# Performance work log

Hardware: AMD Instinct MI355X
Metric: run time of the kernel (lower is better)

## Reference

```python
import jax, jax.numpy as jnp
import numpy as np

H, W = 160, 160
FS = 7
SPAN = FS // 2
NUM_CLASSES = 19
NUM_ITERS = 5
THETA_ALPHA = 160.0  # scales rgb in bilateral features
THETA_BETA = 3.0     # scales position in bilateral features
THETA_GAMMA = 3.0    # scales position in spatial features
EPS = 1e-20

# offsets ordered (dx outer, dy inner) to match TF filter-tap index (dx+span)*FS + (dy+span)
OFFSETS = [(dx, dy) for dx in range(-SPAN, SPAN + 1) for dy in range(-SPAN, SPAN + 1)]


def _make_filter(features):
    # features: (bs, cf, H, W) -> gaussian affinity filter (bs, FS*FS, H, W)
    # filter[b, k, i, j] = exp(-0.5 * ||f[b,:,i+dx,j+dy] - f[b,:,i,j]||^2), 0 if out of bounds
    fp = jnp.pad(features, ((0, 0), (0, 0), (SPAN, SPAN), (SPAN, SPAN)))
    rows = jnp.arange(H)
    cols = jnp.arange(W)
    taps = []
    for dx, dy in OFFSETS:
        shifted = fp[:, :, SPAN + dx:SPAN + dx + H, SPAN + dy:SPAN + dy + W]
        aff = jnp.exp(-0.5 * jnp.sum((features - shifted) ** 2, axis=1))  # (bs, H, W)
        mask = (((rows + dx >= 0) & (rows + dx < H))[:, None]
                & ((cols + dy >= 0) & (cols + dy < W))[None, :])
        taps.append(aff * mask)
    return jnp.stack(taps, axis=1)  # (bs, FS*FS, H, W)


def _patches(x):
    # x: (bs, C, H, W) -> (bs, C, FS*FS, H, W), zero-padded shifts (matches extract_patches SAME)
    xp = jnp.pad(x, ((0, 0), (0, 0), (SPAN, SPAN), (SPAN, SPAN)))
    return jnp.stack(
        [xp[:, :, SPAN + dx:SPAN + dx + H, SPAN + dy:SPAN + dy + W] for dx, dy in OFFSETS],
        axis=2)


def _compute_gaussian(x, filt):
    # x: (bs, C, H, W), filt: (bs, FS*FS, H, W) -> (bs, C, H, W)
    return jnp.sum(_patches(x) * filt[:, None], axis=2)


def _forward(unaries, rgb, spatial_ker_weights, bilateral_ker_weights, compatibility_matrix):
    u = jnp.transpose(unaries, (0, 3, 1, 2))     # (bs, C, H, W)
    rgb_nchw = jnp.transpose(rgb, (0, 3, 1, 2))  # (bs, 3, H, W)
    bs = u.shape[0]
    mesh = jnp.stack(
        jnp.meshgrid(jnp.arange(H, dtype=jnp.float32), jnp.arange(W, dtype=jnp.float32),
                     indexing='ij'), 0)          # (2, H, W)
    spatial_feat = jnp.broadcast_to((mesh / THETA_GAMMA)[None], (bs, 2, H, W))
    bilateral_feat = jnp.concatenate(
        [rgb_nchw / THETA_ALPHA,
         jnp.broadcast_to((mesh / THETA_BETA)[None], (bs, 2, H, W))], axis=1)  # (bs, 5, H, W)

    spatial_filter = _make_filter(spatial_feat)
    bilateral_filter = _make_filter(bilateral_feat)

    ones = jnp.ones_like(u)
    spatial_norm = _compute_gaussian(ones, spatial_filter)
    bilateral_norm = _compute_gaussian(ones, bilateral_filter)

    q = u
    for _ in range(NUM_ITERS):
        # NOTE: original code does tf.nn.softmax(q_values, 0) -> softmax over the BATCH axis.
        sm = jax.nn.softmax(q, axis=0)
        s_out = _compute_gaussian(sm, spatial_filter) / (spatial_norm + EPS)
        b_out = _compute_gaussian(sm, bilateral_filter) / (bilateral_norm + EPS)
        msg = (jnp.einsum('kc,bchw->bkhw', spatial_ker_weights, s_out)
               + jnp.einsum('kc,bchw->bkhw', bilateral_ker_weights, b_out))
        pairwise = jnp.einsum('kc,bchw->bkhw', compatibility_matrix, msg)
        q = u - pairwise
    return jnp.transpose(q, (0, 2, 3, 1))  # (bs, H, W, C)


def setup_inputs() -> dict:
    key = jax.random.key(0)
    k1, k2 = jax.random.split(key)
    unaries = jax.random.normal(k1, (2, H, W, NUM_CLASSES), dtype=jnp.float32)
    rgb = jax.random.uniform(k2, (2, H, W, 3), dtype=jnp.float32) * 255.0
    eye = jnp.eye(NUM_CLASSES, dtype=jnp.float32)
    return {
        'unaries': unaries,
        'rgb': rgb,
        'spatial_ker_weights': eye,            # _diagonal_initializer
        'bilateral_ker_weights': eye,          # _diagonal_initializer
        'compatibility_matrix': -eye,          # _potts_model_initializer
    }


def reference(unaries, rgb, spatial_ker_weights, bilateral_ker_weights, compatibility_matrix):
    return _forward(unaries, rgb, spatial_ker_weights, bilateral_ker_weights,
                    compatibility_matrix)
```

## Files before the change

### kernel.cpp

```cpp
#include <hip/hip_runtime.h>


typedef __attribute__((ext_vector_type(4))) _Float16 half4;
typedef __attribute__((ext_vector_type(2))) _Float16 half2f;
typedef __attribute__((ext_vector_type(4))) float float4v;

#define HH 160
#define WW 160
#define NPIX (HH*WW)
#define NC 19
#define NG 5
#define SPAN 3
#define TR 8
#define TC 16
#define NPXT 128
#define LR 14
#define LC 22
#define LCP 24
#define HSTRIDE (LR*LCP)
#define LCP_F 25
#define HS_F (LR*LCP_F)
#define NHALO (LR*LC)
#define NRING 180
#define NBLK 200
#define NTHR 640
#define EPSF 1e-20f

#define EPTAG   0x5EED0000u
#define EPMASK  0xFFFF0000u

#define EPW(b) (32 + (b)*32)

#define SZ_A    30720
#define OFF_WB  SZ_A
#define PN_OFF  20480
#define SHM_SZ  (SZ_A + 25*128*8)

__device__ __forceinline__ float fast_rcp(float x) { return __builtin_amdgcn_rcpf(x); }

__device__ __forceinline__ float smx0(float q0, float q1) {
    const float m  = fmaxf(q0, q1);
    const float e0 = __expf(q0 - m);
    const float e1 = __expf(q1 - m);
    return e0 * fast_rcp(e0 + e1);
}

__device__ __forceinline__ unsigned ep_decode(unsigned w) {
    return ((w & EPMASK) == EPTAG) ? (w & 0xFFFFu) : 0u;
}

__global__ void __launch_bounds__(NTHR) crf_kernel(
        const float* __restrict__ u,
        const float* __restrict__ rgb,
        const float* __restrict__ sw,
        const float* __restrict__ bw,
        const float* __restrict__ compat,
        unsigned long long* __restrict__ gsmA,
        unsigned long long* __restrict__ gsmB,
        unsigned* __restrict__ bar,
        float* __restrict__ out) {
    __shared__ __align__(16) char shm[SHM_SZ];
    __shared__ float Msh[960];
    __shared__ float rowsum[NC];
    __shared__ int   diagflag;
    float4*   rgbL = (float4*)shm;
    float4v*  smF  = (float4v*)shm;
    float*    accF = (float*)shm;
    unsigned* wbW  = (unsigned*)(shm + OFF_WB);
    const uint2* wbP = (const uint2*)(shm + OFF_WB);

    constexpr float WSPC[49] = {
        0.36787944f,0.48567179f,0.57375342f,0.60653066f,0.57375342f,0.48567179f,0.36787944f,
        0.48567179f,0.64118039f,0.75746513f,0.80073740f,0.75746513f,0.64118039f,0.48567179f,
        0.57375342f,0.75746513f,0.89483932f,0.94595947f,0.89483932f,0.75746513f,0.57375342f,
        0.60653066f,0.80073740f,0.94595947f,1.00000000f,0.94595947f,0.80073740f,0.60653066f,
        0.57375342f,0.75746513f,0.89483932f,0.94595947f,0.89483932f,0.75746513f,0.57375342f,
        0.48567179f,0.64118039f,0.75746513f,0.80073740f,0.75746513f,0.64118039f,0.48567179f,
        0.36787944f,0.48567179f,0.57375342f,0.60653066f,0.57375342f,0.48567179f,0.36787944f };

    const int tid = threadIdx.x;
    const int px  = tid & 127;
    const int g   = tid >> 7;
    const int r   = px >> 4, c = px & 15;
    const int ti0 = blockIdx.y * TR, tj0 = blockIdx.x * TC;
    const int gp  = (ti0 + r) * WW + (tj0 + c);
    const int ctr  = (r + SPAN) * LCP   + (c + SPAN);
    const int ctrF = (r + SPAN) * LCP_F + (c + SPAN);
    const int ku  = 4 * g;
    const int bid = blockIdx.y * 10 + blockIdx.x;

    int nb[8];
    {
        const int bx = blockIdx.x, by = blockIdx.y;
        int k = 0;
        #pragma unroll
        for (int dy2 = -1; dy2 <= 1; ++dy2)
            #pragma unroll
            for (int dx2 = -1; dx2 <= 1; ++dx2) {
                if (dx2 == 0 && dy2 == 0) continue;
                const int nx = bx + dx2, ny = by + dy2;
                nb[k++] = ((unsigned)nx < 10u && (unsigned)ny < 20u) ? (ny*10 + nx) : bid;
            }
    }

    if (tid == 0) diagflag = 1;

    float uv0[4], uv1[4];
    #pragma unroll
    for (int i = 0; i < 4; ++i) {
        const int ch = 4*g + i;
        uv0[i] = (ch < NC) ? u[(size_t)gp * NC + ch] : 0.0f;
        uv1[i] = (ch < NC) ? u[((size_t)NPIX + gp) * NC + ch] : 0.0f;
    }
    half4 sh;
    float smv[4];
    #pragma unroll
    for (int i = 0; i < 4; ++i) {
        smv[i] = smx0(uv0[i], uv1[i]);
        sh[i]  = (_Float16)smv[i];
    }
    {
        unsigned long long u64; __builtin_memcpy(&u64, &sh, 8);
        __hip_atomic_store(&gsmA[g * NPIX + gp], u64,
                           __ATOMIC_RELAXED, __HIP_MEMORY_SCOPE_AGENT);
    }

    if (tid < NC) {
        float rs = 0.0f;
        for (int cb = 0; cb < NC; ++cb) rs += sw[tid*NC + cb] + bw[tid*NC + cb];
        rowsum[tid] = rs;
    }
    __syncthreads();
    if (tid == 0)
        __hip_atomic_store(&bar[EPW(bid)], EPTAG | 1u,
                           __ATOMIC_RELAXED, __HIP_MEMORY_SCOPE_AGENT);

    float4 rv;
    int rgb_idx = -1;
    if (tid < 2 * NHALO) {
        const int bb = tid / NHALO, pos = tid % NHALO;
        const int hr = pos / LC, hc = pos % LC;
        const int yi = ti0 - SPAN + hr, xj = tj0 - SPAN + hc;
        rv = make_float4(0.f, 0.f, 0.f, 0.f);
        if ((unsigned)yi < HH && (unsigned)xj < WW) {
            const float* p = rgb + ((size_t)(bb * NPIX) + yi * WW + xj) * 3;
            rv = make_float4(p[0]*(1.f/160.f), p[1]*(1.f/160.f), p[2]*(1.f/160.f), 1.f);
        }
        rgb_idx = (bb ? HSTRIDE : 0) + hr * LCP + hc;
    }

    for (int e = tid; e < 960; e += NTHR) {
        const int k = e / 48, cc2 = e % 48;
        float acc = 0.0f;
        if (k < NC) {
            if (cc2 < NC) {
                for (int j = 0; j < NC; ++j) acc += compat[k*NC + j] * sw[j*NC + cc2];
            } else if (cc2 >= 20 && cc2 < 20 + NC) {
                const int cb = cc2 - 20;
                for (int j = 0; j < NC; ++j) acc += compat[k*NC + j] * bw[j*NC + cb];
            } else if (cc2 == 40) {
                for (int j = 0; j < NC; ++j) acc += compat[k*NC + j] * rowsum[j];
            }
        }
        Msh[e] = acc;
        bool off = false;
        if (k < NC) {
            if (cc2 < NC && cc2 != k && acc != 0.0f) off = true;
            if (cc2 >= 20 && cc2 < 20 + NC && (cc2 - 20) != k && acc != 0.0f) off = true;
        }
        if (off) atomicAnd(&diagflag, 0);
    }

    if (rgb_idx >= 0) rgbL[rgb_idx] = rv;
    __syncthreads();

    float dsv[4], dbv[4];
    #pragma unroll
    for (int i = 0; i < 4; ++i) {
        dsv[i] = Msh[(ku + i) * 48 + (ku + i)];
        dbv[i] = Msh[(ku + i) * 48 + 20 + (ku + i)];
    }
    const bool isdiag = (diagflag != 0);

    {
        const float4 cv0 = rgbL[ctr];
        const float4 cv1 = rgbL[HSTRIDE + ctr];
        const int tapb = g * 10;
        const int ntap = (g == 4) ? 9 : 10;
        float pn0 = 0.f, pn1 = 0.f;
        for (int i = 0; i < ntap; ++i) {
            const int t = tapb + i;
            const int dx = t / 7 - SPAN, dy = t % 7 - SPAN;
            const int n = ctr + dx * LCP + dy;
            const float4 nv0 = rgbL[n];
            const float4 nv1 = rgbL[HSTRIDE + n];
            const float spc = (float)(dx*dx + dy*dy) * (-1.f/18.f);
            const float dr0 = cv0.x-nv0.x, dg0 = cv0.y-nv0.y, db0 = cv0.z-nv0.z;
            const float dr1 = cv1.x-nv1.x, dg1 = cv1.y-nv1.y, db1 = cv1.z-nv1.z;
            const float d0 = dr0*dr0 + dg0*dg0 + db0*db0;
            const float d1 = dr1*dr1 + dg1*dg1 + db1*db1;
            const float wb0 = nv0.w * __expf(fmaf(d0, -0.5f, spc));
            const float wb1 = nv0.w * __expf(fmaf(d1, -0.5f, spc));
            half2f hw = {(_Float16)wb0, (_Float16)wb1};
            unsigned uw; __builtin_memcpy(&uw, &hw, 4);
            wbW[(t >> 1) * 256 + px * 2 + (t & 1)] = uw;
            pn0 += (float)hw.x; pn1 += (float)hw.y;
        }
        if (g == 4) wbW[24 * 256 + px * 2 + 1] = 0u;
        *(float2*)(shm + PN_OFF + (g * 128 + px) * 8) = make_float2(pn0, pn1);
    }
    __syncthreads();

    float snI, bnI0, bnI1;
    {
        float bn0 = 0.f, bn1 = 0.f;
        #pragma unroll
        for (int g2 = 0; g2 < 5; ++g2) {
            const float2 p = *(const float2*)(shm + PN_OFF + (g2 * 128 + px) * 8);
            bn0 += p.x; bn1 += p.y;
        }
        const int rg = ti0 + r, cg = tj0 + c;
        float Rr = 5.70645506f, Cc = 5.70645506f;
        Rr -= (rg < 3   ? 0.60653066f : 0.f) + (rg < 2   ? 0.80073740f : 0.f)
            + (rg < 1   ? 0.94595947f : 0.f) + (rg > 156 ? 0.60653066f : 0.f)
            + (rg > 157 ? 0.80073740f : 0.f) + (rg > 158 ? 0.94595947f : 0.f);
        Cc -= (cg < 3   ? 0.60653066f : 0.f) + (cg < 2   ? 0.80073740f : 0.f)
            + (cg < 1   ? 0.94595947f : 0.f) + (cg > 156 ? 0.60653066f : 0.f)
            + (cg > 157 ? 0.80073740f : 0.f) + (cg > 158 ? 0.94595947f : 0.f);
        snI  = fast_rcp(Rr * Cc + EPSF);
        bnI0 = fast_rcp(bn0 + EPSF);
        bnI1 = fast_rcp(bn1 + EPSF);
    }

    for (int it = 0; it < 5; ++it) {
        __syncthreads();

        {
            const float4v sv = {smv[0], smv[1], smv[2], smv[3]};
            smF[g * HS_F + ctrF] = sv;
        }

        if (tid == 0) {
            const unsigned seq = (unsigned)(it + 1);
            if (it > 0)
                __hip_atomic_store(&bar[EPW(bid)], EPTAG | seq,
                                   __ATOMIC_RELAXED, __HIP_MEMORY_SCOPE_AGENT);
            unsigned mn;
            do {
                mn = 0xFFFFu;
                #pragma unroll
                for (int k = 0; k < 8; ++k) {
                    const unsigned w = __hip_atomic_load(&bar[EPW(nb[k])],
                                                         __ATOMIC_RELAXED, __HIP_MEMORY_SCOPE_AGENT);
                    const unsigned e = ep_decode(w);
                    mn = (e < mn) ? e : mn;
                }
                if (mn < seq) __builtin_amdgcn_s_sleep(1);
            } while (mn < seq);
        }
        __syncthreads();

        const unsigned long long* gsrc = ((it & 1) ? gsmB : gsmA);
        #pragma unroll
        for (int k2 = 0; k2 < 2; ++k2) {
            const int e = tid + NTHR * k2;
            if (e < NG * NRING) {
                const int sg = e / NRING, re = e - sg * NRING;
                int hr, hc;
                if (re < 66)        { hr = re / 22;          hc = re % 22; }
                else if (re < 132)  { const int t2 = re - 66;  hr = 11 + t2 / 22; hc = t2 % 22; }
                else                { const int t2 = re - 132; hr = 3 + t2 / 6;
                                      const int s = t2 % 6;    hc = (s < 3) ? s : s + 16; }
                const int yi = ti0 - SPAN + hr, xj = tj0 - SPAN + hc;
                float4v fv = (float4v)0.0f;
                if ((unsigned)yi < HH && (unsigned)xj < WW) {
                    const unsigned long long raw =
                        __hip_atomic_load(&gsrc[sg * NPIX + yi * WW + xj],
                                          __ATOMIC_RELAXED, __HIP_MEMORY_SCOPE_AGENT);
                    half4 hv; __builtin_memcpy(&hv, &raw, 8);
                    fv = (float4v){(float)hv[0], (float)hv[1], (float)hv[2], (float)hv[3]};
                }
                smF[sg * HS_F + hr * LCP_F + hc] = fv;
            }
        }
        __syncthreads();

        float4v sAv = (float4v)0.0f, b0a = (float4v)0.0f, b1a = (float4v)0.0f;
        const float4v* pl = smF + g * HS_F;
        #pragma unroll
        for (int i = 0; i < 24; ++i) {
            const uint2 wp = wbP[i * 128 + px];
            #pragma unroll
            for (int s = 0; s < 2; ++s) {
                const int t = 2*i + s;
                const int dx = t / 7 - SPAN, dy = t % 7 - SPAN;
                half2f hw; __builtin_memcpy(&hw, s ? &wp.y : &wp.x, 4);
                const float w0 = (float)hw.x, w1 = (float)hw.y;
                const float4v f = pl[ctrF + dx*LCP_F + dy];
                sAv += WSPC[t] * f;
                b0a += w0 * f;
                b1a += w1 * f;
            }
        }
        {
            const uint2 wp = wbP[24 * 128 + px];
            half2f hw; __builtin_memcpy(&hw, &wp.x, 4);
            const float w0 = (float)hw.x, w1 = (float)hw.y;
            const float4v f = pl[ctrF + SPAN*LCP_F + SPAN];
            sAv += WSPC[48] * f;
            b0a += w0 * f;
            b1a += w1 * f;
        }

        float q0v[4], q1v[4];
        if (isdiag) {
            #pragma unroll
            for (int i = 0; i < 4; ++i) {
                const float sAn = sAv[i] * snI;
                const float b0n = b0a[i] * bnI0;
                const float b1x = b1a[i] * bnI1;
                q0v[i] = uv0[i] - dsv[i]*sAn - dbv[i]*b0n;
                q1v[i] = uv1[i] - (dsv[i] + dbv[i]) + dsv[i]*sAn + dbv[i]*b1x;
            }
        } else {
            __syncthreads();
            #pragma unroll
            for (int i = 0; i < 4; ++i) {
                accF[(4*g + i) * NPXT + px]      = sAv[i] * snI;
                accF[(20 + 4*g + i) * NPXT + px] = b0a[i] * bnI0;
                accF[(40 + 4*g + i) * NPXT + px] = b1a[i] * bnI1;
            }
            __syncthreads();
            float t1[4] = {0,0,0,0}, t2[4] = {0,0,0,0}, t3[4] = {0,0,0,0};
            #pragma unroll
            for (int cc = 0; cc < 20; ++cc) {
                const float sv  = accF[cc * NPXT + px];
                const float b0v = accF[(20 + cc) * NPXT + px];
                const float b1v = accF[(40 + cc) * NPXT + px];
                #pragma unroll
                for (int i = 0; i < 4; ++i) {
                    const float* mk = Msh + (ku + i) * 48;
                    t1[i] += mk[cc] * sv;
                    t2[i] += mk[20 + cc] * b0v;
                    t3[i] += mk[20 + cc] * b1v;
                }
            }
            #pragma unroll
            for (int i = 0; i < 4; ++i) {
                const float rs = Msh[(ku + i) * 48 + 40];
                q0v[i] = uv0[i] - t1[i] - t2[i];
                q1v[i] = uv1[i] - rs + t1[i] + t3[i];
            }
        }

        if (it == 4) {
            #pragma unroll
            for (int i = 0; i < 4; ++i) {
                const int ch = 4*g + i;
                if (ch < NC) {
                    out[(size_t)gp * NC + ch]          = q0v[i];
                    out[((size_t)NPIX + gp) * NC + ch] = q1v[i];
                }
            }
        } else {
            #pragma unroll
            for (int i = 0; i < 4; ++i) {
                smv[i] = smx0(q0v[i], q1v[i]);
                sh[i]  = (_Float16)smv[i];
            }
            unsigned long long u64; __builtin_memcpy(&u64, &sh, 8);
            unsigned long long* gdst = (((it + 1) & 1) ? gsmB : gsmA);
            __hip_atomic_store(&gdst[g * NPIX + gp], u64,
                               __ATOMIC_RELAXED, __HIP_MEMORY_SCOPE_AGENT);
        }
    }
}

extern "C" void kernel_launch(void* const* d_in, const int* in_sizes, int n_in,
                              void* d_out, int out_size, void* d_ws, size_t ws_size,
                              hipStream_t stream) {
    const float* u      = (const float*)d_in[0];
    const float* rgb    = (const float*)d_in[1];
    const float* sw     = (const float*)d_in[2];
    const float* bw     = (const float*)d_in[3];
    const float* compat = (const float*)d_in[4];
    float* out = (float*)d_out;

    unsigned long long* gsmA = (unsigned long long*)d_ws;
    unsigned long long* gsmB = (unsigned long long*)((char*)d_ws + 1024000);
    unsigned* bar = (unsigned*)((char*)d_ws + 2048000);

    crf_kernel<<<dim3(WW/TC, HH/TR, 1), dim3(NTHR), 0, stream>>>(
        u, rgb, sw, bw, compat, gsmA, gsmB, bar, out);
}
```

Measured before the change: 101.9 us.

## Retile to 10x10 pixel blocks over a 16x16 grid of 256 blocks

Changes the spatial tile from 8x16 to 10x10 pixels, giving 256 persistent blocks of 512 threads (500 active) instead of 200 blocks of 640. The halo, ring-exchange indexing, shared-memory strides and neighbour barrier are adjusted to match. The intent is to fill all 256 CUs of the MI355X so each neighbour-synchronized iteration finishes sooner. In exchange the halo-to-interior ratio rises, 12 threads per block sit idle, and the barrier spin now gives up after a bounded count, which could break the synchronization if a neighbour is very slow.

```diff
diff --git a/kernel.cpp b/kernel.cpp
--- a/kernel.cpp
+++ b/kernel.cpp
@@ -11,19 +11,18 @@
 #define NC 19
 #define NG 5
 #define SPAN 3
-#define TR 8
-#define TC 16
-#define NPXT 128
-#define LR 14
-#define LC 22
-#define LCP 24
+#define TR 10
+#define TC 10
+#define NPXT 100
+#define LR 16
+#define LC 16
+#define LCP 17
 #define HSTRIDE (LR*LCP)
-#define LCP_F 25
-#define HS_F (LR*LCP_F)
 #define NHALO (LR*LC)
-#define NRING 180
-#define NBLK 200
-#define NTHR 640
+#define NRING 156
+#define NBLK 256
+#define NTHR 512
+#define NACT 500
 #define EPSF 1e-20f
 
 #define EPTAG   0x5EED0000u
@@ -31,10 +30,10 @@
 
 #define EPW(b) (32 + (b)*32)
 
-#define SZ_A    30720
+#define SZ_A    24064
+#define PN_OFF  8704
 #define OFF_WB  SZ_A
-#define PN_OFF  20480
-#define SHM_SZ  (SZ_A + 25*128*8)
+#define SHM_SZ  (SZ_A + 20000)
 
 __device__ __forceinline__ float fast_rcp(float x) { return __builtin_amdgcn_rcpf(x); }
 
@@ -79,15 +78,15 @@
         0.36787944f,0.48567179f,0.57375342f,0.60653066f,0.57375342f,0.48567179f,0.36787944f };
 
     const int tid = threadIdx.x;
-    const int px  = tid & 127;
-    const int g   = tid >> 7;
-    const int r   = px >> 4, c = px & 15;
+    const bool act = (tid < NACT);
+    const int g   = tid / NPXT;
+    const int px  = tid - g * NPXT;
+    const int r   = px / TC, c = px - r * TC;
     const int ti0 = blockIdx.y * TR, tj0 = blockIdx.x * TC;
     const int gp  = (ti0 + r) * WW + (tj0 + c);
-    const int ctr  = (r + SPAN) * LCP   + (c + SPAN);
-    const int ctrF = (r + SPAN) * LCP_F + (c + SPAN);
+    const int ctr = (r + SPAN) * LCP + (c + SPAN);
     const int ku  = 4 * g;
-    const int bid = blockIdx.y * 10 + blockIdx.x;
+    const int bid = blockIdx.y * 16 + blockIdx.x;
 
     int nb[8];
     {
@@ -99,27 +98,27 @@
             for (int dx2 = -1; dx2 <= 1; ++dx2) {
                 if (dx2 == 0 && dy2 == 0) continue;
                 const int nx = bx + dx2, ny = by + dy2;
-                nb[k++] = ((unsigned)nx < 10u && (unsigned)ny < 20u) ? (ny*10 + nx) : bid;
+                nb[k++] = ((unsigned)nx < 16u && (unsigned)ny < 16u) ? (ny*16 + nx) : bid;
             }
     }
 
     if (tid == 0) diagflag = 1;
 
     float uv0[4], uv1[4];
-    #pragma unroll
-    for (int i = 0; i < 4; ++i) {
-        const int ch = 4*g + i;
-        uv0[i] = (ch < NC) ? u[(size_t)gp * NC + ch] : 0.0f;
-        uv1[i] = (ch < NC) ? u[((size_t)NPIX + gp) * NC + ch] : 0.0f;
-    }
     half4 sh;
     float smv[4];
-    #pragma unroll
-    for (int i = 0; i < 4; ++i) {
-        smv[i] = smx0(uv0[i], uv1[i]);
-        sh[i]  = (_Float16)smv[i];
-    }
-    {
+    if (act) {
+        #pragma unroll
+        for (int i = 0; i < 4; ++i) {
+            const int ch = 4*g + i;
+            uv0[i] = (ch < NC) ? u[(size_t)gp * NC + ch] : 0.0f;
+            uv1[i] = (ch < NC) ? u[((size_t)NPIX + gp) * NC + ch] : 0.0f;
+        }
+        #pragma unroll
+        for (int i = 0; i < 4; ++i) {
+            smv[i] = smx0(uv0[i], uv1[i]);
+            sh[i]  = (_Float16)smv[i];
+        }
         unsigned long long u64; __builtin_memcpy(&u64, &sh, 8);
         __hip_atomic_store(&gsmA[g * NPIX + gp], u64,
                            __ATOMIC_RELAXED, __HIP_MEMORY_SCOPE_AGENT);
@@ -136,17 +135,17 @@
                            __ATOMIC_RELAXED, __HIP_MEMORY_SCOPE_AGENT);
 
     float4 rv;
-    int rgb_idx = -1;
-    if (tid < 2 * NHALO) {
-        const int bb = tid / NHALO, pos = tid % NHALO;
-        const int hr = pos / LC, hc = pos % LC;
+    int rgb_idx;
+    {
+        const int bb = tid >> 8, pos = tid & 255;
+        const int hr = pos >> 4, hc = pos & 15;
         const int yi = ti0 - SPAN + hr, xj = tj0 - SPAN + hc;
         rv = make_float4(0.f, 0.f, 0.f, 0.f);
         if ((unsigned)yi < HH && (unsigned)xj < WW) {
             const float* p = rgb + ((size_t)(bb * NPIX) + yi * WW + xj) * 3;
             rv = make_float4(p[0]*(1.f/160.f), p[1]*(1.f/160.f), p[2]*(1.f/160.f), 1.f);
         }
-        rgb_idx = (bb ? HSTRIDE : 0) + hr * LCP + hc;
+        rgb_idx = bb * HSTRIDE + hr * LCP + hc;
     }
 
     for (int e = tid; e < 960; e += NTHR) {
@@ -171,7 +170,7 @@
         if (off) atomicAnd(&diagflag, 0);
     }
 
-    if (rgb_idx >= 0) rgbL[rgb_idx] = rv;
+    rgbL[rgb_idx] = rv;
     __syncthreads();
 
     float dsv[4], dbv[4];
@@ -182,7 +181,7 @@
     }
     const bool isdiag = (diagflag != 0);
 
-    {
+    if (act) {
         const float4 cv0 = rgbL[ctr];
         const float4 cv1 = rgbL[HSTRIDE + ctr];
         const int tapb = g * 10;
@@ -203,20 +202,20 @@
             const float wb1 = nv0.w * __expf(fmaf(d1, -0.5f, spc));
             half2f hw = {(_Float16)wb0, (_Float16)wb1};
             unsigned uw; __builtin_memcpy(&uw, &hw, 4);
-            wbW[(t >> 1) * 256 + px * 2 + (t & 1)] = uw;
+            wbW[(t >> 1) * 200 + px * 2 + (t & 1)] = uw;
             pn0 += (float)hw.x; pn1 += (float)hw.y;
         }
-        if (g == 4) wbW[24 * 256 + px * 2 + 1] = 0u;
-        *(float2*)(shm + PN_OFF + (g * 128 + px) * 8) = make_float2(pn0, pn1);
+        if (g == 4) wbW[24 * 200 + px * 2 + 1] = 0u;
+        *(float2*)(shm + PN_OFF + (g * NPXT + px) * 8) = make_float2(pn0, pn1);
     }
     __syncthreads();
 
     float snI, bnI0, bnI1;
-    {
+    if (act) {
         float bn0 = 0.f, bn1 = 0.f;
         #pragma unroll
         for (int g2 = 0; g2 < 5; ++g2) {
-            const float2 p = *(const float2*)(shm + PN_OFF + (g2 * 128 + px) * 8);
+            const float2 p = *(const float2*)(shm + PN_OFF + (g2 * NPXT + px) * 8);
             bn0 += p.x; bn1 += p.y;
         }
         const int rg = ti0 + r, cg = tj0 + c;
@@ -235,9 +234,9 @@
     for (int it = 0; it < 5; ++it) {
         __syncthreads();
 
-        {
+        if (act) {
             const float4v sv = {smv[0], smv[1], smv[2], smv[3]};
-            smF[g * HS_F + ctrF] = sv;
+            smF[g * HSTRIDE + ctr] = sv;
         }
 
         if (tid == 0) {
@@ -246,6 +245,7 @@
                 __hip_atomic_store(&bar[EPW(bid)], EPTAG | seq,
                                    __ATOMIC_RELAXED, __HIP_MEMORY_SCOPE_AGENT);
             unsigned mn;
+            unsigned spins = 0;
             do {
                 mn = 0xFFFFu;
                 #pragma unroll
@@ -255,7 +255,10 @@
                     const unsigned e = ep_decode(w);
                     mn = (e < mn) ? e : mn;
                 }
-                if (mn < seq) __builtin_amdgcn_s_sleep(1);
+                if (mn < seq) {
+                    __builtin_amdgcn_s_sleep(1);
+                    if (++spins > (1u << 22)) break;
+                }
             } while (mn < seq);
         }
         __syncthreads();
@@ -267,10 +270,10 @@
             if (e < NG * NRING) {
                 const int sg = e / NRING, re = e - sg * NRING;
                 int hr, hc;
-                if (re < 66)        { hr = re / 22;          hc = re % 22; }
-                else if (re < 132)  { const int t2 = re - 66;  hr = 11 + t2 / 22; hc = t2 % 22; }
-                else                { const int t2 = re - 132; hr = 3 + t2 / 6;
-                                      const int s = t2 % 6;    hc = (s < 3) ? s : s + 16; }
+                if (re < 48)        { hr = re >> 4;               hc = re & 15; }
+                else if (re < 96)   { hr = 13 + ((re - 48) >> 4); hc = (re - 48) & 15; }
+                else                { const int t2 = re - 96; hr = 3 + t2 / 6;
+                                      const int s = t2 % 6;   hc = (s < 3) ? s : s + 10; }
                 const int yi = ti0 - SPAN + hr, xj = tj0 - SPAN + hc;
                 float4v fv = (float4v)0.0f;
                 if ((unsigned)yi < HH && (unsigned)xj < WW) {
@@ -280,89 +283,99 @@
                     half4 hv; __builtin_memcpy(&hv, &raw, 8);
                     fv = (float4v){(float)hv[0], (float)hv[1], (float)hv[2], (float)hv[3]};
                 }
-                smF[sg * HS_F + hr * LCP_F + hc] = fv;
+                smF[sg * HSTRIDE + hr * LCP + hc] = fv;
             }
         }
         __syncthreads();
 
         float4v sAv = (float4v)0.0f, b0a = (float4v)0.0f, b1a = (float4v)0.0f;
-        const float4v* pl = smF + g * HS_F;
-        #pragma unroll
-        for (int i = 0; i < 24; ++i) {
-            const uint2 wp = wbP[i * 128 + px];
+        if (act) {
+            const float4v* pl = smF + g * HSTRIDE;
             #pragma unroll
-            for (int s = 0; s < 2; ++s) {
-                const int t = 2*i + s;
-                const int dx = t / 7 - SPAN, dy = t % 7 - SPAN;
-                half2f hw; __builtin_memcpy(&hw, s ? &wp.y : &wp.x, 4);
+            for (int i = 0; i < 24; ++i) {
+                const uint2 wp = wbP[i * 100 + px];
+                #pragma unroll
+                for (int s = 0; s < 2; ++s) {
+                    const int t = 2*i + s;
+                    const int dx = t / 7 - SPAN, dy = t % 7 - SPAN;
+                    half2f hw; __builtin_memcpy(&hw, s ? &wp.y : &wp.x, 4);
+                    const float w0 = (float)hw.x, w1 = (float)hw.y;
+                    const float4v f = pl[ctr + dx*LCP + dy];
+                    sAv += WSPC[t] * f;
+                    b0a += w0 * f;
+                    b1a += w1 * f;
+                }
+            }
+            {
+                const uint2 wp = wbP[24 * 100 + px];
+                half2f hw; __builtin_memcpy(&hw, &wp.x, 4);
                 const float w0 = (float)hw.x, w1 = (float)hw.y;
-                const float4v f = pl[ctrF + dx*LCP_F + dy];
-                sAv += WSPC[t] * f;
+                const float4v f = pl[ctr + SPAN*LCP + SPAN];
+                sAv += WSPC[48] * f;
                 b0a += w0 * f;
                 b1a += w1 * f;
             }
         }
-        {
-            const uint2 wp = wbP[24 * 128 + px];
-            half2f hw; __builtin_memcpy(&hw, &wp.x, 4);
-            const float w0 = (float)hw.x, w1 = (float)hw.y;
-            const float4v f = pl[ctrF + SPAN*LCP_F + SPAN];
-            sAv += WSPC[48] * f;
-            b0a += w0 * f;
-            b1a += w1 * f;
-        }
 
         float q0v[4], q1v[4];
         if (isdiag) {
-            #pragma unroll
-            for (int i = 0; i < 4; ++i) {
-                const float sAn = sAv[i] * snI;
-                const float b0n = b0a[i] * bnI0;
-                const float b1x = b1a[i] * bnI1;
-                q0v[i] = uv0[i] - dsv[i]*sAn - dbv[i]*b0n;
-                q1v[i] = uv1[i] - (dsv[i] + dbv[i]) + dsv[i]*sAn + dbv[i]*b1x;
+            if (act) {
+                #pragma unroll
+                for (int i = 0; i < 4; ++i) {
+                    const float sAn = sAv[i] * snI;
+                    const float b0n = b0a[i] * bnI0;
+                    const float b1x = b1a[i] * bnI1;
+                    q0v[i] = uv0[i] - dsv[i]*sAn - dbv[i]*b0n;
+                    q1v[i] = uv1[i] - (dsv[i] + dbv[i]) + dsv[i]*sAn + dbv[i]*b1x;
+                }
             }
         } else {
             __syncthreads();
-            #pragma unroll
-            for (int i = 0; i < 4; ++i) {
-                accF[(4*g + i) * NPXT + px]      = sAv[i] * snI;
-                accF[(20 + 4*g + i) * NPXT + px] = b0a[i] * bnI0;
-                accF[(40 + 4*g + i) * NPXT + px] = b1a[i] * bnI1;
+            if (act) {
+                #pragma unroll
+                for (int i = 0; i < 4; ++i) {
+                    accF[(4*g + i) * NPXT + px]      = sAv[i] * snI;
+                    accF[(20 + 4*g + i) * NPXT + px] = b0a[i] * bnI0;
+                    accF[(40 + 4*g + i) * NPXT + px] = b1a[i] * bnI1;
+                }
             }
             __syncthreads();
-            float t1[4] = {0,0,0,0}, t2[4] = {0,0,0,0}, t3[4] = {0,0,0,0};
-            #pragma unroll
-            for (int cc = 0; cc < 20; ++cc) {
-                const float sv  = accF[cc * NPXT + px];
-                const float b0v = accF[(20 + cc) * NPXT + px];
-                const float b1v = accF[(40 + cc) * NPXT + px];
+            if (act) {
+                float t1[4] = {0,0,0,0}, t2[4] = {0,0,0,0}, t3[4] = {0,0,0,0};
+                #pragma unroll
+                for (int cc = 0; cc < 20; ++cc) {
+                    const float sv  = accF[cc * NPXT + px];
+                    const float b0v = accF[(20 + cc) * NPXT + px];
+                    const float b1v = accF[(40 + cc) * NPXT + px];
+                    #pragma unroll
+                    for (int i = 0; i < 4; ++i) {
+                        const float* mk = Msh + (ku + i) * 48;
+                        t1[i] += mk[cc] * sv;
+                        t2[i] += mk[20 + cc] * b0v;
+                        t3[i] += mk[20 + cc] * b1v;
+                    }
+                }
                 #pragma unroll
                 for (int i = 0; i < 4; ++i) {
-                    const float* mk = Msh + (ku + i) * 48;
-                    t1[i] += mk[cc] * sv;
-                    t2[i] += mk[20 + cc] * b0v;
-                    t3[i] += mk[20 + cc] * b1v;
-                }
-            }
-            #pragma unroll
-            for (int i = 0; i < 4; ++i) {
-                const float rs = Msh[(ku + i) * 48 + 40];
-                q0v[i] = uv0[i] - t1[i] - t2[i];
-                q1v[i] = uv1[i] - rs + t1[i] + t3[i];
+                    const float rs = Msh[(ku + i) * 48 + 40];
+                    q0v[i] = uv0[i] - t1[i] - t2[i];
+                    q1v[i] = uv1[i] - rs + t1[i] + t3[i];
+                }
             }
         }
 
         if (it == 4) {
-            #pragma unroll
-            for (int i = 0; i < 4; ++i) {
-                const int ch = 4*g + i;
-                if (ch < NC) {
-                    out[(size_t)gp * NC + ch]          = q0v[i];
-                    out[((size_t)NPIX + gp) * NC + ch] = q1v[i];
-                }
-            }
-        } else {
+            if (act) {
+                #pragma unroll
+                for (int i = 0; i < 4; ++i) {
+                    const int ch = 4*g + i;
+                    if (ch < NC) {
+                        out[(size_t)gp * NC + ch]          = q0v[i];
+                        out[((size_t)NPIX + gp) * NC + ch] = q1v[i];
+                    }
+                }
+            }
+        } else if (act) {
             #pragma unroll
             for (int i = 0; i < 4; ++i) {
                 smv[i] = smx0(q0v[i], q1v[i]);
```

Result: faster. 98.13 us (-3.7%).
